# Kernel optimization log

Measured on AMD Instinct MI355X. Metric: run time of the kernel, lower is better.

## Reference

```python
import jax, jax.numpy as jnp
import numpy as np

B, T, V, H, L = 32, 256, 32000, 512, 2

def setup_inputs() -> dict:
    key = jax.random.key(0)
    ks = jax.random.split(key, 6)
    scale = 1.0 / np.sqrt(H)
    tokens = jax.random.randint(ks[0], (B, T), 0, V)
    lengths = jax.random.randint(ks[1], (B,), T // 2, T + 1)
    embedding = jax.random.normal(ks[2], (V, H), jnp.float32) * scale
    Wx = jax.random.normal(ks[3], (L, H, 4 * H), jnp.float32) * scale
    Wh = jax.random.normal(ks[4], (L, H, 4 * H), jnp.float32) * scale
    b = jnp.zeros((L, 4 * H), jnp.float32)
    return {"tokens": tokens, "lengths": lengths, "embedding": embedding,
            "Wx": Wx, "Wh": Wh, "b": b}

def _lstm_layer(x, lengths, Wx, Wh, b):
    # x: [B, T, H]; length-masked carry (state frozen once t >= length)
    Bb, Tt, Hh = x.shape
    def step(carry, inp):
        c, h = carry
        xt, t = inp
        z = xt @ Wx + h @ Wh + b            # [B, 4H]
        i, f, g, o = jnp.split(z, 4, axis=-1)
        nc = jax.nn.sigmoid(f) * c + jax.nn.sigmoid(i) * jnp.tanh(g)
        nh = jax.nn.sigmoid(o) * jnp.tanh(nc)
        mask = (t < lengths)[:, None]
        c = jnp.where(mask, nc, c)
        h = jnp.where(mask, nh, h)
        return (c, h), h
    init = (jnp.zeros((Bb, Hh), x.dtype), jnp.zeros((Bb, Hh), x.dtype))
    (c, h), ys = jax.lax.scan(step, init, (jnp.swapaxes(x, 0, 1), jnp.arange(Tt)))
    return jnp.swapaxes(ys, 0, 1), (c, h)  # [B, T, H], ([B,H],[B,H])

def reference(tokens, lengths, embedding, Wx, Wh, b):
    x = embedding[tokens]                    # [B, T, H]
    final = None
    for l in range(Wx.shape[0]):             # small fixed layer loop
        x, final = _lstm_layer(x, lengths, Wx[l], Wh[l], b[l])
    # encoder returns (all outputs of top layer, final state of top layer)
    return x, final
```

## Files before the change

kernel.cpp:

```cpp
#include <hip/hip_runtime.h>

#define BB 32
#define TT 256
#define HH 512
#define ALD 1032
#define ZLD 68
#define FLGSTRIDE 32
#define GRIDN 512

typedef float    f32x4 __attribute__((ext_vector_type(4)));
typedef float    f32x2 __attribute__((ext_vector_type(2)));
typedef int      i32x4 __attribute__((ext_vector_type(4)));
typedef _Float16 f16x8 __attribute__((ext_vector_type(8)));
typedef unsigned long long u64;

__device__ __forceinline__ unsigned short f2h(float f) {
  union { _Float16 h; unsigned short u; } v; v.h = (_Float16)f; return v.u;
}
__device__ __forceinline__ int pkh2(float a, float b) {
  return (int)((unsigned int)f2h(a) | ((unsigned int)f2h(b) << 16));
}
__device__ __forceinline__ float sigm(float x) { return 1.f / (1.f + __expf(-x)); }
__device__ __forceinline__ float tanh_(float x) {
  float ax = fabsf(x);
  float e = __expf(-2.f * ax);
  float r = (1.f - e) / (1.f + e);
  return copysignf(r, x);
}
__device__ __forceinline__ void ld_coh16(i32x4& dst, const void* a) {
  asm volatile("global_load_dwordx4 %0, %1, off sc1" : "=v"(dst) : "v"(a) : "memory");
}
__device__ __forceinline__ void ld_l2_16(i32x4& dst, const void* a) {
  asm volatile("global_load_dwordx4 %0, %1, off sc0" : "=v"(dst) : "v"(a) : "memory");
}
__device__ __forceinline__ void st_l2_8(void* a, u64 v) {
  asm volatile("global_store_dwordx2 %0, %1, off" :: "v"(a), "v"(v) : "memory");
}

__global__ void zero_ws_kernel(unsigned int* p, int nwords) {
  int i = blockIdx.x * 256 + threadIdx.x;
  if (i < nwords) p[i] = 0u;
}

__global__ __launch_bounds__(256, 1) void lstm_enc_kernel(
    const int* __restrict__ tokens,
    const int* __restrict__ lengths,
    const float* __restrict__ emb,
    const float* __restrict__ Wx,
    const float* __restrict__ Wh,
    const float* __restrict__ bias,
    float* __restrict__ out,
    unsigned short* __restrict__ ws_y,
    u64* __restrict__ htagL,
    u64* __restrict__ htagG,
    unsigned int* __restrict__ flags,
    unsigned int* __restrict__ ctl)
{
  const int tid = threadIdx.x;

  __shared__ int sRole;
  if (tid == 0) {
    unsigned int xcc;
    asm volatile("s_getreg_b32 %0, hwreg(HW_REG_XCC_ID)" : "=s"(xcc));
    xcc &= 7u;
    if (blockIdx.x == 0) {
      __hip_atomic_store(&ctl[0], 0x100u | xcc, __ATOMIC_RELAXED, __HIP_MEMORY_SCOPE_AGENT);
    }
    unsigned int hw;
    while ((((hw = __hip_atomic_load(&ctl[0], __ATOMIC_RELAXED, __HIP_MEMORY_SCOPE_AGENT))) & 0x100u) == 0u) {
      __builtin_amdgcn_s_sleep(1);
    }
    const unsigned int home0 = hw & 7u, home1 = (home0 + 1u) & 7u;
    int role = -1;
    if (xcc == home0) {
      unsigned int i = __hip_atomic_fetch_add(&ctl[32], 1u, __ATOMIC_RELAXED, __HIP_MEMORY_SCOPE_AGENT);
      if (i < 32u) role = (int)i;
    } else if (xcc == home1) {
      unsigned int i = __hip_atomic_fetch_add(&ctl[64], 1u, __ATOMIC_RELAXED, __HIP_MEMORY_SCOPE_AGENT);
      if (i < 32u) role = 32 + (int)i;
    }
    if (role < 0) {
      unsigned int cl = 0; int spins = 0;
      while ((cl = __hip_atomic_load(&ctl[96], __ATOMIC_RELAXED, __HIP_MEMORY_SCOPE_AGENT)) < 64u
             && spins < 20000) { __builtin_amdgcn_s_sleep(2); ++spins; }
      if (cl < 64u) {
        unsigned int i = __hip_atomic_fetch_add(&ctl[32], 1u, __ATOMIC_RELAXED, __HIP_MEMORY_SCOPE_AGENT);
        if (i < 32u) role = (int)i;
        else {
          unsigned int j = __hip_atomic_fetch_add(&ctl[64], 1u, __ATOMIC_RELAXED, __HIP_MEMORY_SCOPE_AGENT);
          if (j < 32u) role = 32 + (int)j;
        }
      }
    }
    if (role >= 0)
      __hip_atomic_fetch_add(&ctl[96], 1u, __ATOMIC_RELAXED, __HIP_MEMORY_SCOPE_AGENT);
    sRole = role;
  }
  __syncthreads();
  const int role = sRole;
  if (role < 0) return;
  const int layer = role >> 5;
  const int lblk  = role & 31;
  const int wave  = tid >> 6;
  const int lane  = tid & 63;

  __shared__ unsigned short Alds[32 * ALD];
  __shared__ float zlds[32 * ZLD];

  const int nloc  = lane & 15;
  const int gcol  = wave * HH + lblk * 16 + nloc;
  const int krow0 = (lane >> 4) * 8;
  const float* WxL = Wx + (size_t)layer * HH * 2048;
  const float* WhL = Wh + (size_t)layer * HH * 2048;
  f16x8 breg[32];
#pragma unroll
  for (int s = 0; s < 32; ++s) {
    const float* base = (s < 16)
        ? (WxL + (size_t)(s * 32 + krow0) * 2048 + gcol)
        : (WhL + (size_t)((s - 16) * 32 + krow0) * 2048 + gcol);
    f16x8 v;
    v[0] = (_Float16)base[0 * 2048];
    v[1] = (_Float16)base[1 * 2048];
    v[2] = (_Float16)base[2 * 2048];
    v[3] = (_Float16)base[3 * 2048];
    v[4] = (_Float16)base[4 * 2048];
    v[5] = (_Float16)base[5 * 2048];
    v[6] = (_Float16)base[6 * 2048];
    v[7] = (_Float16)base[7 * 2048];
    breg[s] = v;
  }

  const int jj  = tid & 7;
  const int eb  = tid >> 3;
  const int u0  = lblk * 16 + 2 * jj;
  const int len = lengths[eb];
  const float bI0 = bias[layer * 2048 +         u0], bI1 = bias[layer * 2048 +         u0 + 1];
  const float bF0 = bias[layer * 2048 +  512 +  u0], bF1 = bias[layer * 2048 +  512 +  u0 + 1];
  const float bG0 = bias[layer * 2048 + 1024 +  u0], bG1 = bias[layer * 2048 + 1024 +  u0 + 1];
  const float bO0 = bias[layer * 2048 + 1536 +  u0], bO1 = bias[layer * 2048 + 1536 +  u0 + 1];
  float cA = 0.f, hA = 0.f, cB = 0.f, hB = 0.f;

  u64* hlayL = htagL + (size_t)layer * 2 * BB * 256;
  u64* hlayG = htagG + (size_t)layer * 2 * BB * 256;
  unsigned int* pollL0 = flags + (size_t)(tid & 31) * FLGSTRIDE;
  bool useG = false;

  if (layer == 0) {
#pragma unroll
    for (int i = 0; i < 8; ++i) {
      int u   = tid + i * 256;
      int row = u >> 6;
      int ce  = (u & 63) * 8;
      int tok = tokens[row * TT + 0];
      const float* src = emb + (size_t)tok * HH + ce;
      f32x4 lo = *(const f32x4*)src;
      f32x4 hi = *(const f32x4*)(src + 4);
      i32x4 w;
      w[0] = pkh2(lo[0], lo[1]); w[1] = pkh2(lo[2], lo[3]);
      w[2] = pkh2(hi[0], hi[1]); w[3] = pkh2(hi[2], hi[3]);
      *(i32x4*)(&Alds[row * ALD + ce]) = w;
    }
  }

  for (int it = 0;; ++it) {
    const int t = (layer == 0) ? it : (it - 1);
    const bool active = (t >= 0) && (t < TT);

    if (layer == 1 && active) {
      const unsigned int tgt = (unsigned int)(t + 1);
      if (tid < 32) {
        while (__hip_atomic_load(pollL0, __ATOMIC_RELAXED, __HIP_MEMORY_SCOPE_AGENT) < tgt) {
          __builtin_amdgcn_s_sleep(1);
        }
      }
      __syncthreads();
      i32x4 yv[8];
      int yrow[8], yco[8];
#pragma unroll
      for (int k = 0; k < 8; ++k) {
        int g = tid + k * 256;
        yrow[k] = g >> 6;
        yco[k]  = (g & 63) * 8;
        ld_coh16(yv[k], ws_y + ((size_t)yrow[k] * TT + t) * HH + yco[k]);
      }
      asm volatile("s_waitcnt vmcnt(0)" ::: "memory");
      __builtin_amdgcn_sched_barrier(0);
#pragma unroll
      for (int k = 0; k < 8; ++k) {
        *(i32x4*)(&Alds[yrow[k] * ALD + yco[k]]) = yv[k];
      }
    }

    if (active) {
      const u64* srcL = hlayL + (size_t)(t & 1) * BB * 256;
      const u64* srcG = hlayG + (size_t)(t & 1) * BB * 256;
      const unsigned int exp = (unsigned int)t;
      i32x4 hv[16];
      int rounds = 0;
      bool ok = false;
      while (!ok) {
        if (useG) {
#pragma unroll
          for (int k = 0; k < 16; ++k) ld_coh16(hv[k], srcG + 2 * (tid + k * 256));
        } else {
#pragma unroll
          for (int k = 0; k < 16; ++k) ld_l2_16(hv[k], srcL + 2 * (tid + k * 256));
        }
        asm volatile("s_waitcnt vmcnt(0)" ::: "memory");
        __builtin_amdgcn_sched_barrier(0);
        ok = true;
#pragma unroll
        for (int k = 0; k < 16; ++k) {
          if ((unsigned int)hv[k][1] != exp) ok = false;
          if ((unsigned int)hv[k][3] != exp) ok = false;
        }
        if (!ok && ++rounds > 48) useG = true;
      }
#pragma unroll
      for (int k = 0; k < 16; ++k) {
        int g   = tid + k * 256;
        int row = g >> 7;
        int e   = 4 * (g & 127);
        u64 d = (u64)(unsigned int)hv[k][0] | ((u64)(unsigned int)hv[k][2] << 32);
        *(u64*)(&Alds[row * ALD + 512 + e]) = d;
      }
    }
    __syncthreads();

    if (active) {
      f32x4 acc0 = {0.f, 0.f, 0.f, 0.f};
      f32x4 acc1 = {0.f, 0.f, 0.f, 0.f};
      const _Float16* a0p = (const _Float16*)&Alds[nloc * ALD + krow0];
      const _Float16* a1p = a0p + 16 * ALD;
#pragma unroll
      for (int s = 0; s < 32; ++s) {
        f16x8 a0 = *(const f16x8*)(a0p + s * 32);
        f16x8 a1 = *(const f16x8*)(a1p + s * 32);
        acc0 = __builtin_amdgcn_mfma_f32_16x16x32_f16(a0, breg[s], acc0, 0, 0, 0);
        acc1 = __builtin_amdgcn_mfma_f32_16x16x32_f16(a1, breg[s], acc1, 0, 0, 0);
      }
      const int zc = wave * 16 + nloc;
      const int zr = (lane >> 4) * 4;
#pragma unroll
      for (int r = 0; r < 4; ++r) {
        zlds[(zr + r) * ZLD + zc]        = acc0[r];
        zlds[(16 + zr + r) * ZLD + zc]   = acc1[r];
      }
    }
    __syncthreads();

    if (active) {
      float zi0 = zlds[eb * ZLD +      2 * jj] + bI0, zi1 = zlds[eb * ZLD +      2 * jj + 1] + bI1;
      float zf0 = zlds[eb * ZLD + 16 + 2 * jj] + bF0, zf1 = zlds[eb * ZLD + 16 + 2 * jj + 1] + bF1;
      float zg0 = zlds[eb * ZLD + 32 + 2 * jj] + bG0, zg1 = zlds[eb * ZLD + 32 + 2 * jj + 1] + bG1;
      float zo0 = zlds[eb * ZLD + 48 + 2 * jj] + bO0, zo1 = zlds[eb * ZLD + 48 + 2 * jj + 1] + bO1;
      float ncA = sigm(zf0) * cA + sigm(zi0) * tanh_(zg0);
      float nhA = sigm(zo0) * tanh_(ncA);
      float ncB = sigm(zf1) * cB + sigm(zi1) * tanh_(zg1);
      float nhB = sigm(zo1) * tanh_(ncB);
      if (t < len) { cA = ncA; hA = nhA; cB = ncB; hB = nhB; }
      unsigned int hp = (unsigned int)f2h(hA) | ((unsigned int)f2h(hB) << 16);
      u64 hv2 = ((u64)(unsigned int)(t + 1) << 32) | (u64)hp;
      const size_t hoff = (size_t)((t + 1) & 1) * BB * 256 + eb * 256 + lblk * 8 + jj;
      st_l2_8(&hlayL[hoff], hv2);
      __hip_atomic_store(&hlayG[hoff], hv2, __ATOMIC_RELAXED, __HIP_MEMORY_SCOPE_AGENT);
      if (layer == 0) {
        __hip_atomic_store((unsigned int*)(ws_y + ((size_t)eb * TT + t) * HH + u0), hp,
                           __ATOMIC_RELAXED, __HIP_MEMORY_SCOPE_AGENT);
      } else {
        f32x2 o; o[0] = hA; o[1] = hB;
        *(f32x2*)(out + ((size_t)eb * TT + t) * HH + u0) = o;
      }
    }

    if (it == TT) break;

    if (layer == 0) {
      __syncthreads();
      if (tid == 0 && active) {
        __hip_atomic_store(flags + (size_t)lblk * FLGSTRIDE, (unsigned int)(it + 1),
                           __ATOMIC_RELAXED, __HIP_MEMORY_SCOPE_AGENT);
      }
      const int tn = it + 1;
      if (tn < TT) {
#pragma unroll
        for (int i = 0; i < 8; ++i) {
          int u   = tid + i * 256;
          int row = u >> 6;
          int ce  = (u & 63) * 8;
          int tok = tokens[row * TT + tn];
          const float* src = emb + (size_t)tok * HH + ce;
          f32x4 lo = *(const f32x4*)src;
          f32x4 hi = *(const f32x4*)(src + 4);
          i32x4 w;
          w[0] = pkh2(lo[0], lo[1]); w[1] = pkh2(lo[2], lo[3]);
          w[2] = pkh2(hi[0], hi[1]); w[3] = pkh2(hi[2], hi[3]);
          *(i32x4*)(&Alds[row * ALD + ce]) = w;
        }
      }
    }
  }

  if (layer == 1) {
    const size_t coff = (size_t)BB * TT * HH;
    const size_t hoff = coff + (size_t)BB * HH;
    f32x2 c2; c2[0] = cA; c2[1] = cB;
    f32x2 h2; h2[0] = hA; h2[1] = hB;
    *(f32x2*)(out + coff + (size_t)eb * HH + u0) = c2;
    *(f32x2*)(out + hoff + (size_t)eb * HH + u0) = h2;
  }
}

extern "C" void kernel_launch(void* const* d_in, const int* in_sizes, int n_in,
                              void* d_out, int out_size, void* d_ws, size_t ws_size,
                              hipStream_t stream) {
  (void)in_sizes; (void)n_in; (void)out_size; (void)ws_size;
  const int* tokens  = (const int*)d_in[0];
  const int* lengths = (const int*)d_in[1];
  const float* emb   = (const float*)d_in[2];
  const float* Wx    = (const float*)d_in[3];
  const float* Wh    = (const float*)d_in[4];
  const float* bias  = (const float*)d_in[5];

  char* w = (char*)d_ws;
  const size_t FB = (size_t)32 * FLGSTRIDE * 4;
  const size_t CT = 512;
  const size_t HT = (size_t)2 * 2 * BB * 256 * 8;
  unsigned int*   flags = (unsigned int*)w;
  unsigned int*   ctl   = (unsigned int*)(w + FB);
  u64*            htagL = (u64*)(w + FB + CT);
  u64*            htagG = (u64*)(w + FB + CT + HT);
  unsigned short* ws_y  = (unsigned short*)(w + FB + CT + 2 * HT);

  const int zero_words = (int)((FB + CT + 2 * HT) / 4);
  hipLaunchKernelGGL(zero_ws_kernel, dim3((zero_words + 255) / 256), dim3(256), 0, stream,
                     (unsigned int*)d_ws, zero_words);
  hipLaunchKernelGGL(lstm_enc_kernel, dim3(GRIDN), dim3(256), 0, stream,
                     tokens, lengths, emb, Wx, Wh, bias, (float*)d_out,
                     ws_y, htagL, htagG, flags, ctl);
}
```

Baseline: 1.620 ms.

## Poll per-block L2 step flags before loading tagged hidden state; split MFMA accumulators

Each layer's blocks now publish a per-block step counter into a new L2-local flag array. Before loading the tagged hidden-state buffer, the first 32 threads spin on those 32 flags with short sleeps, so the block issues one bulk load once all producers are done instead of repeatedly reloading 16 vectors per thread. The recurrent MFMA chain is also split into two independent accumulators per tile to shorten the dependency chain. The cost is an extra flag store, an extra barrier per step and more workspace, and the flag poll adds latency if flags propagate slower than the data.

```diff
diff --git a/kernel.cpp b/kernel.cpp
--- a/kernel.cpp
+++ b/kernel.cpp
@@ -33,8 +33,17 @@
 __device__ __forceinline__ void ld_l2_16(i32x4& dst, const void* a) {
   asm volatile("global_load_dwordx4 %0, %1, off sc0" : "=v"(dst) : "v"(a) : "memory");
 }
+__device__ __forceinline__ unsigned int ld_l2_4(const void* a) {
+  unsigned int v;
+  asm volatile("global_load_dword %0, %1, off sc0" : "=v"(v) : "v"(a) : "memory");
+  asm volatile("s_waitcnt vmcnt(0)" ::: "memory");
+  return v;
+}
 __device__ __forceinline__ void st_l2_8(void* a, u64 v) {
   asm volatile("global_store_dwordx2 %0, %1, off" :: "v"(a), "v"(v) : "memory");
+}
+__device__ __forceinline__ void st_l2_4(void* a, unsigned int v) {
+  asm volatile("global_store_dword %0, %1, off" :: "v"(a), "v"(v) : "memory");
 }
 
 __global__ void zero_ws_kernel(unsigned int* p, int nwords) {
@@ -54,6 +63,7 @@
     u64* __restrict__ htagL,
     u64* __restrict__ htagG,
     unsigned int* __restrict__ flags,
+    unsigned int* __restrict__ flagsL,
     unsigned int* __restrict__ ctl)
 {
   const int tid = threadIdx.x;
@@ -142,7 +152,9 @@
 
   u64* hlayL = htagL + (size_t)layer * 2 * BB * 256;
   u64* hlayG = htagG + (size_t)layer * 2 * BB * 256;
-  unsigned int* pollL0 = flags + (size_t)(tid & 31) * FLGSTRIDE;
+  unsigned int* pollL0  = flags + (size_t)(tid & 31) * FLGSTRIDE;
+  unsigned int* pollLoc = flagsL + (size_t)(layer * 32 + (tid & 31)) * FLGSTRIDE;
+  unsigned int* myFlagL = flagsL + (size_t)(layer * 32 + lblk) * FLGSTRIDE;
   bool useG = false;
 
   if (layer == 0) {
@@ -192,12 +204,26 @@
     }
 
     if (active) {
+      const unsigned int tgtF = (unsigned int)t;
+      if (tid < 32) {
+        while (ld_l2_4(pollLoc) < tgtF) __builtin_amdgcn_s_sleep(1);
+      }
+      __syncthreads();
       const u64* srcL = hlayL + (size_t)(t & 1) * BB * 256;
       const u64* srcG = hlayG + (size_t)(t & 1) * BB * 256;
       const unsigned int exp = (unsigned int)t;
       i32x4 hv[16];
+#pragma unroll
+      for (int k = 0; k < 16; ++k) ld_l2_16(hv[k], srcL + 2 * (tid + k * 256));
+      asm volatile("s_waitcnt vmcnt(0)" ::: "memory");
+      __builtin_amdgcn_sched_barrier(0);
+      bool ok = true;
+#pragma unroll
+      for (int k = 0; k < 16; ++k) {
+        if ((unsigned int)hv[k][1] != exp) ok = false;
+        if ((unsigned int)hv[k][3] != exp) ok = false;
+      }
       int rounds = 0;
-      bool ok = false;
       while (!ok) {
         if (useG) {
 #pragma unroll
@@ -228,23 +254,30 @@
     __syncthreads();
 
     if (active) {
-      f32x4 acc0 = {0.f, 0.f, 0.f, 0.f};
-      f32x4 acc1 = {0.f, 0.f, 0.f, 0.f};
+      f32x4 acc0a = {0.f,0.f,0.f,0.f}, acc0b = {0.f,0.f,0.f,0.f};
+      f32x4 acc1a = {0.f,0.f,0.f,0.f}, acc1b = {0.f,0.f,0.f,0.f};
       const _Float16* a0p = (const _Float16*)&Alds[nloc * ALD + krow0];
       const _Float16* a1p = a0p + 16 * ALD;
 #pragma unroll
-      for (int s = 0; s < 32; ++s) {
+      for (int s = 0; s < 16; ++s) {
         f16x8 a0 = *(const f16x8*)(a0p + s * 32);
         f16x8 a1 = *(const f16x8*)(a1p + s * 32);
-        acc0 = __builtin_amdgcn_mfma_f32_16x16x32_f16(a0, breg[s], acc0, 0, 0, 0);
-        acc1 = __builtin_amdgcn_mfma_f32_16x16x32_f16(a1, breg[s], acc1, 0, 0, 0);
+        acc0a = __builtin_amdgcn_mfma_f32_16x16x32_f16(a0, breg[s], acc0a, 0, 0, 0);
+        acc1a = __builtin_amdgcn_mfma_f32_16x16x32_f16(a1, breg[s], acc1a, 0, 0, 0);
+      }
+#pragma unroll
+      for (int s = 16; s < 32; ++s) {
+        f16x8 a0 = *(const f16x8*)(a0p + s * 32);
+        f16x8 a1 = *(const f16x8*)(a1p + s * 32);
+        acc0b = __builtin_amdgcn_mfma_f32_16x16x32_f16(a0, breg[s], acc0b, 0, 0, 0);
+        acc1b = __builtin_amdgcn_mfma_f32_16x16x32_f16(a1, breg[s], acc1b, 0, 0, 0);
       }
       const int zc = wave * 16 + nloc;
       const int zr = (lane >> 4) * 4;
 #pragma unroll
       for (int r = 0; r < 4; ++r) {
-        zlds[(zr + r) * ZLD + zc]        = acc0[r];
-        zlds[(16 + zr + r) * ZLD + zc]   = acc1[r];
+        zlds[(zr + r) * ZLD + zc]        = acc0a[r] + acc0b[r];
+        zlds[(16 + zr + r) * ZLD + zc]   = acc1a[r] + acc1b[r];
       }
     }
     __syncthreads();
@@ -275,12 +308,15 @@
 
     if (it == TT) break;
 
-    if (layer == 0) {
-      __syncthreads();
-      if (tid == 0 && active) {
+    __syncthreads();
+    if (tid == 0 && active) {
+      st_l2_4(myFlagL, (unsigned int)(t + 1));
+      if (layer == 0) {
         __hip_atomic_store(flags + (size_t)lblk * FLGSTRIDE, (unsigned int)(it + 1),
                            __ATOMIC_RELAXED, __HIP_MEMORY_SCOPE_AGENT);
       }
+    }
+    if (layer == 0) {
       const int tn = it + 1;
       if (tn < TT) {
 #pragma unroll
@@ -323,19 +359,21 @@
   const float* bias  = (const float*)d_in[5];
 
   char* w = (char*)d_ws;
-  const size_t FB = (size_t)32 * FLGSTRIDE * 4;
-  const size_t CT = 512;
-  const size_t HT = (size_t)2 * 2 * BB * 256 * 8;
-  unsigned int*   flags = (unsigned int*)w;
-  unsigned int*   ctl   = (unsigned int*)(w + FB);
-  u64*            htagL = (u64*)(w + FB + CT);
-  u64*            htagG = (u64*)(w + FB + CT + HT);
-  unsigned short* ws_y  = (unsigned short*)(w + FB + CT + 2 * HT);
-
-  const int zero_words = (int)((FB + CT + 2 * HT) / 4);
+  const size_t FB  = (size_t)32 * FLGSTRIDE * 4;
+  const size_t CT  = 512;
+  const size_t FLB = (size_t)64 * FLGSTRIDE * 4;
+  const size_t HT  = (size_t)2 * 2 * BB * 256 * 8;
+  unsigned int*   flags  = (unsigned int*)w;
+  unsigned int*   ctl    = (unsigned int*)(w + FB);
+  unsigned int*   flagsL = (unsigned int*)(w + FB + CT);
+  u64*            htagL  = (u64*)(w + FB + CT + FLB);
+  u64*            htagG  = (u64*)(w + FB + CT + FLB + HT);
+  unsigned short* ws_y   = (unsigned short*)(w + FB + CT + FLB + 2 * HT);
+
+  const int zero_words = (int)((FB + CT + FLB + 2 * HT) / 4);
   hipLaunchKernelGGL(zero_ws_kernel, dim3((zero_words + 255) / 256), dim3(256), 0, stream,
                      (unsigned int*)d_ws, zero_words);
   hipLaunchKernelGGL(lstm_enc_kernel, dim3(GRIDN), dim3(256), 0, stream,
                      tokens, lengths, emb, Wx, Wh, bias, (float*)d_out,
-                     ws_y, htagL, htagG, flags, ctl);
-}
+                     ws_y, htagL, htagG, flags, flagsL, ctl);
+}
```

After: 1.655 ms. 2.2% more time.
